# Performance work log

Hardware: AMD Instinct MI355X
Metric: run time of the kernel (lower is better)

The kernel has to match this reference:

```python
import jax, jax.numpy as jnp
import numpy as np

N_NODES = 1000
N_EDGES = 8000
IN_FEATS = 64
HID = 128
RDIM = HID // 2  # UniversalReadout output dim
EPS = 1e-5


def _lrelu(v):
    return jax.nn.leaky_relu(v, 0.01)


def setup_inputs() -> dict:
    key = jax.random.key(0)
    ks = jax.random.split(key, 16)
    B = 128
    node_feats = jax.random.normal(ks[0], (B * N_NODES, IN_FEATS), jnp.float32)
    edge_weights = jax.random.uniform(ks[1], (B * N_EDGES,), jnp.float32)
    g_weights = jax.random.uniform(ks[2], (B * N_NODES,), jnp.float32)
    src = jax.random.randint(ks[3], (N_EDGES,), 0, N_NODES)
    dst = jax.random.randint(ks[4], (N_EDGES,), 0, N_NODES)
    # GraphConv weights (in, out), kaiming-ish scale
    W1 = jax.random.normal(ks[5], (IN_FEATS, HID), jnp.float32) / np.sqrt(IN_FEATS)
    W2 = jax.random.normal(ks[6], (HID, HID), jnp.float32) / np.sqrt(HID)
    W3 = jax.random.normal(ks[7], (HID, HID), jnp.float32) / np.sqrt(HID)
    suppl = jnp.ones((3, N_EDGES), jnp.float32)           # suppl_weights_conv1..3
    AR = jnp.ones((4, N_NODES), jnp.float32)              # AR1..AR4 weights
    gn_gamma = jnp.ones((3, HID), jnp.float32)
    gn_beta = jnp.zeros((3, HID), jnp.float32)
    gn_alpha = jnp.ones((3, HID), jnp.float32)            # GraphNorm mean-scale
    phi_W = jax.random.normal(ks[8], (3, HID, HID), jnp.float32) / np.sqrt(HID)
    phi_b = jnp.zeros((3, HID), jnp.float32)
    rho_W = jax.random.normal(ks[9], (3, HID, RDIM), jnp.float32) / np.sqrt(HID)
    rho_b = jnp.zeros((3, RDIM), jnp.float32)
    return dict(node_feats=node_feats, edge_weights=edge_weights, g_weights=g_weights,
                W1=W1, W2=W2, W3=W3, suppl=suppl, AR=AR,
                gn_gamma=gn_gamma, gn_beta=gn_beta, gn_alpha=gn_alpha,
                phi_W=phi_W, phi_b=phi_b, rho_W=rho_W, rho_b=rho_b,
                src=src, dst=dst)


def _forward(node_feats, edge_weights, g_weights, W1, W2, W3, suppl, AR,
             gn_gamma, gn_beta, gn_alpha, phi_W, phi_b, rho_W, rho_b, src, dst):
    B = node_feats.shape[0] // N_NODES
    x = node_feats.reshape(B, N_NODES, -1)        # (B, N, F)
    gw = g_weights.reshape(B, N_NODES)            # (B, N)
    ew = edge_weights.reshape(B, N_EDGES)         # (B, E)

    # structural degree normalization (norm='both'), shared topology
    deg_out = jnp.maximum(jnp.zeros((N_NODES,), x.dtype).at[src].add(1.0), 1.0)
    deg_in = jnp.maximum(jnp.zeros((N_NODES,), x.dtype).at[dst].add(1.0), 1.0)
    n_out = deg_out ** -0.5
    n_in = deg_in ** -0.5

    def gconv(h, W, ew_l):
        hs = h * n_out[None, :, None]
        msgs = hs[:, src, :] * ew_l[:, :, None]                       # (B, E, D)
        agg = jnp.zeros_like(hs).at[:, dst].add(msgs)                  # scatter-add
        return (agg * n_in[None, :, None]) @ W

    def gnorm(h, i):
        mean = h.mean(axis=1, keepdims=True)
        sub = h - gn_alpha[i] * mean
        var = (sub * sub).mean(axis=1, keepdims=True)
        return gn_gamma[i] * sub * jax.lax.rsqrt(var + EPS) + gn_beta[i]

    def uro(h, i):  # UniversalReadout (deep-sets): per-node MLP -> sum -> MLP
        z = _lrelu(h @ phi_W[i] + phi_b[i]).sum(axis=1)
        return _lrelu(z @ rho_W[i] + rho_b[i])

    def wmean(h, ar):  # dgl.mean_nodes with node weight: mean over nodes of w*x
        w = gw * ar[None, :]
        return (w[:, :, None] * h).mean(axis=1)

    pieces = [wmean(x, AR[0])]
    h = x
    Ws = (W1, W2, W3)
    for i in range(3):
        h = _lrelu(gnorm(gconv(h, Ws[i], ew * suppl[i][None, :]), i))
        pieces.append(uro(h, i))
        pieces.append(wmean(h, AR[i + 1]))
    return _lrelu(jnp.concatenate(pieces, axis=-1))


def reference(node_feats, edge_weights, g_weights, W1, W2, W3, suppl, AR,
              gn_gamma, gn_beta, gn_alpha, phi_W, phi_b, rho_W, rho_b, src, dst):
    return _forward(node_feats, edge_weights, g_weights, W1, W2, W3, suppl, AR,
                    gn_gamma, gn_beta, gn_alpha, phi_W, phi_b, rho_W, rho_b, src, dst)
```

## Files before the change

### kernel.cpp

```cpp
#include <hip/hip_runtime.h>
#include <cstddef>

#define NN 1000
#define NE 8000
#define FIN 64
#define DH 128
#define RD 64
#define FEPS 1e-5f

typedef short short8 __attribute__((ext_vector_type(8)));
typedef float f32x4 __attribute__((ext_vector_type(4)));

__device__ __forceinline__ float lrelu(float x){ return x > 0.f ? x : 0.01f*x; }

__device__ __forceinline__ unsigned short f2b(float x){
  union { float f; unsigned int u; } v; v.f = x;
  unsigned int r = (v.u + 0x7fffu + ((v.u >> 16) & 1u)) >> 16;
  return (unsigned short)r;
}
__device__ __forceinline__ float b2f(unsigned int lo16){
  union { unsigned int u; float f; } v; v.u = lo16 << 16; return v.f;
}
__device__ __forceinline__ unsigned int pack2(float a, float b){
  return (unsigned int)f2b(a) | ((unsigned int)f2b(b) << 16);
}


__global__ __launch_bounds__(1024) void k_prep(const int* __restrict__ src,
        const int* __restrict__ dst,
        const float* __restrict__ W1, const float* __restrict__ W2,
        const float* __restrict__ W3, const float* __restrict__ phiW,
        unsigned short* __restrict__ wt,
        const float* __restrict__ x, const float* __restrict__ gw,
        const float* __restrict__ AR, float* __restrict__ out,
        float* nout, float* nin, int* rp, int* ord,
        int* csr_s, int* csr_e, int* csr_d, int B){
  __shared__ int sdo[1024], sdi[1024], ssc[1024], sfill[1024];
  __shared__ int hist[256], hoff[256];
  __shared__ float red2[16][64];
  int bid = blockIdx.x, t = threadIdx.x;

  if (bid == 0){
    sdo[t] = 0; sdi[t] = 0;
    __syncthreads();
    for (int e = t; e < NE; e += 1024){
      atomicAdd(&sdo[src[e]], 1);
      atomicAdd(&sdi[dst[e]], 1);
    }
    __syncthreads();
    int d = sdi[t];
    ssc[t] = d; __syncthreads();
    for (int off = 1; off < 1024; off <<= 1){
      int v = (t >= off) ? ssc[t-off] : 0;
      __syncthreads();
      ssc[t] += v;
      __syncthreads();
    }
    int myrp = ssc[t] - d;
    if (t < NN){
      rp[t] = myrp;
      nin[t]  = rsqrtf((float)max(sdi[t], 1));
      nout[t] = rsqrtf((float)max(sdo[t], 1));
    }
    if (t == NN-1) rp[NN] = ssc[t];
    sfill[t] = myrp;
    __syncthreads();
    for (int e = t; e < NE; e += 1024){
      int dn = dst[e];
      int pos = atomicAdd(&sfill[dn], 1);
      csr_s[pos] = src[e];
      csr_e[pos] = e;
      csr_d[pos] = dn;
    }
    if (t < 256) hist[t] = 0;
    __syncthreads();
    if (t < NN) atomicAdd(&hist[min(sdi[t], 255)], 1);
    __syncthreads();
    if (t < 256) hoff[t] = hist[t];
    __syncthreads();
    for (int off = 1; off < 256; off <<= 1){
      int v = (t < 256 && t >= off) ? hoff[t-off] : 0;
      __syncthreads();
      if (t < 256) hoff[t] += v;
      __syncthreads();
    }
    if (t < 256) hoff[t] -= hist[t];
    __syncthreads();
    if (t < NN){
      int pos = atomicAdd(&hoff[min(sdi[t], 255)], 1);
      ord[pos] = t;
    }
  } else if (bid <= 88){
    int i = (bid-1)*1024 + t;
    if (i < 8192){
      int n = i >> 6, k = i & 63;
      wt[i] = f2b(W1[k*128 + n]);
    } else if (i < 24576){
      int j = i - 8192; int n = j >> 7, k = j & 127;
      wt[i] = f2b(W2[k*128 + n]);
    } else if (i < 40960){
      int j = i - 24576; int n = j >> 7, k = j & 127;
      wt[i] = f2b(W3[k*128 + n]);
    } else {
      int j = i - 40960; int m = j >> 14; int jj = j & 16383;
      int n = jj >> 7, k = jj & 127;
      wt[i] = f2b(phiW[m*16384 + k*128 + n]);
    }
  } else {
    int b = bid - 89;
    int r = t >> 6, l = t & 63;
    float acc = 0.f;
    for (int v = r; v < NN; v += 16)
      acc += gw[(size_t)b*NN + v]*AR[v]*x[((size_t)b*NN + v)*FIN + l];
    red2[r][l] = acc;
    __syncthreads();
    if (t < 64){
      float s = 0.f;
      #pragma unroll
      for (int g2 = 0; g2 < 16; ++g2) s += red2[g2][t];
      out[(size_t)b*640 + t] = s*(1.f/NN);
    }
  }
}


__global__ __launch_bounds__(256) void k_edge(const float* __restrict__ ew,
        const float* __restrict__ sup, const float* __restrict__ nout,
        const float* __restrict__ nin, const int* __restrict__ csr_s,
        const int* __restrict__ csr_e, const int* __restrict__ csr_d,
        int2* __restrict__ ecl, float* __restrict__ statz, int nz4, int B){
  int bid = blockIdx.x, t = threadIdx.x;
  int gi = bid*256 + t;
  if (gi < nz4) ((float4*)statz)[gi] = make_float4(0.f,0.f,0.f,0.f);
  int layer, b, q;
  if ((B & 7) == 0){
    int xcd = bid & 7, r = bid >> 3;
    int bsub = r/12, rem = r - bsub*12;
    layer = rem >> 2; q = rem & 3; b = bsub*8 + xcd;
  } else {
    layer = bid/(4*B);
    int rem = bid - layer*4*B;
    b = rem >> 2; q = rem & 3;
  }
  const float* ewb  = ew  + (size_t)b*NE;
  const float* supl = sup + (size_t)layer*NE;
  int2* o = ecl + ((size_t)layer*B + b)*NE;
  for (int k = q*2000 + t; k < q*2000 + 2000; k += 256){
    int e = csr_e[k]; int s = csr_s[k];
    float wv = ewb[e]*supl[e]*nout[s]*nin[csr_d[k]];
    int2 v; v.x = s; v.y = __float_as_int(wv);
    o[k] = v;
  }
}


__global__ __launch_bounds__(256) void k_gathF(const float* __restrict__ x,
        const int2* __restrict__ ec, const int* __restrict__ rp,
        const int* __restrict__ ord, unsigned short* __restrict__ agg, int B){
  int bid = blockIdx.x;
  int b, chunk;
  if ((B & 7) == 0){
    int xcd = bid & 7, r = bid >> 3;
    int bsub = r/63; chunk = r - bsub*63; b = bsub*8 + xcd;
  } else { b = bid/63; chunk = bid - b*63; }
  int t = threadIdx.x;
  int grp = t >> 4, j = t & 15;
  int rk = chunk*16 + grp; if (rk > NN-1) rk = NN-1;
  int v = ord[rk];
  int kb = rp[v], ke = rp[v+1];
  const float* xb = x + (size_t)b*NN*FIN;
  const int2* ecb = ec + (size_t)b*NE;
  float acc[4][4] = {};
  int k = kb;
  for (; k+3 < ke; k += 4){
    #pragma unroll
    for (int uu = 0; uu < 4; ++uu){
      int2 e = ecb[k+uu];
      float4 xr = *(const float4*)(xb + e.x*FIN + j*4);
      float wgt = __int_as_float(e.y);
      acc[uu][0] = fmaf(xr.x, wgt, acc[uu][0]);
      acc[uu][1] = fmaf(xr.y, wgt, acc[uu][1]);
      acc[uu][2] = fmaf(xr.z, wgt, acc[uu][2]);
      acc[uu][3] = fmaf(xr.w, wgt, acc[uu][3]);
    }
  }
  for (; k < ke; ++k){
    int2 e = ecb[k];
    float4 xr = *(const float4*)(xb + e.x*FIN + j*4);
    float wgt = __int_as_float(e.y);
    acc[0][0] = fmaf(xr.x, wgt, acc[0][0]);
    acc[0][1] = fmaf(xr.y, wgt, acc[0][1]);
    acc[0][2] = fmaf(xr.z, wgt, acc[0][2]);
    acc[0][3] = fmaf(xr.w, wgt, acc[0][3]);
  }
  uint2 o;
  o.x = pack2(acc[0][0]+acc[1][0]+acc[2][0]+acc[3][0],
              acc[0][1]+acc[1][1]+acc[2][1]+acc[3][1]);
  o.y = pack2(acc[0][2]+acc[1][2]+acc[2][2]+acc[3][2],
              acc[0][3]+acc[1][3]+acc[2][3]+acc[3][3]);
  *(uint2*)(agg + ((size_t)b*NN + v)*FIN + j*4) = o;
}


__global__ __launch_bounds__(256) void k_gathB(const unsigned short* __restrict__ h,
        const int2* __restrict__ ec, const int* __restrict__ rp,
        const int* __restrict__ ord, unsigned short* __restrict__ agg, int B){
  int bid = blockIdx.x;
  int b, chunk;
  if ((B & 7) == 0){
    int xcd = bid & 7, r = bid >> 3;
    int bsub = r/63; chunk = r - bsub*63; b = bsub*8 + xcd;
  } else { b = bid/63; chunk = bid - b*63; }
  int t = threadIdx.x;
  int grp = t >> 4, j = t & 15;
  int rk = chunk*16 + grp; if (rk > NN-1) rk = NN-1;
  int v = ord[rk];
  int kb = rp[v], ke = rp[v+1];
  const unsigned short* hb = h + (size_t)b*NN*DH;
  const int2* ecb = ec + (size_t)b*NE;
  float acc[4][8] = {};
  int k = kb;
  for (; k+3 < ke; k += 4){
    #pragma unroll
    for (int uu = 0; uu < 4; ++uu){
      int2 e = ecb[k+uu];
      uint4 u = *(const uint4*)(hb + e.x*DH + j*8);
      float wgt = __int_as_float(e.y);
      acc[uu][0] = fmaf(b2f(u.x & 0xffffu), wgt, acc[uu][0]);
      acc[uu][1] = fmaf(b2f(u.x >> 16),     wgt, acc[uu][1]);
      acc[uu][2] = fmaf(b2f(u.y & 0xffffu), wgt, acc[uu][2]);
      acc[uu][3] = fmaf(b2f(u.y >> 16),     wgt, acc[uu][3]);
      acc[uu][4] = fmaf(b2f(u.z & 0xffffu), wgt, acc[uu][4]);
      acc[uu][5] = fmaf(b2f(u.z >> 16),     wgt, acc[uu][5]);
      acc[uu][6] = fmaf(b2f(u.w & 0xffffu), wgt, acc[uu][6]);
      acc[uu][7] = fmaf(b2f(u.w >> 16),     wgt, acc[uu][7]);
    }
  }
  for (; k < ke; ++k){
    int2 e = ecb[k];
    uint4 u = *(const uint4*)(hb + e.x*DH + j*8);
    float wgt = __int_as_float(e.y);
    acc[0][0] = fmaf(b2f(u.x & 0xffffu), wgt, acc[0][0]);
    acc[0][1] = fmaf(b2f(u.x >> 16),     wgt, acc[0][1]);
    acc[0][2] = fmaf(b2f(u.y & 0xffffu), wgt, acc[0][2]);
    acc[0][3] = fmaf(b2f(u.y >> 16),     wgt, acc[0][3]);
    acc[0][4] = fmaf(b2f(u.z & 0xffffu), wgt, acc[0][4]);
    acc[0][5] = fmaf(b2f(u.z >> 16),     wgt, acc[0][5]);
    acc[0][6] = fmaf(b2f(u.w & 0xffffu), wgt, acc[0][6]);
    acc[0][7] = fmaf(b2f(u.w >> 16),     wgt, acc[0][7]);
  }
  float f[8];
  #pragma unroll
  for (int d2 = 0; d2 < 8; ++d2)
    f[d2] = acc[0][d2]+acc[1][d2]+acc[2][d2]+acc[3][d2];
  uint4 o;
  o.x = pack2(f[0],f[1]); o.y = pack2(f[2],f[3]);
  o.z = pack2(f[4],f[5]); o.w = pack2(f[6],f[7]);
  *(uint4*)(agg + ((size_t)b*NN + v)*DH + j*8) = o;
}


template<int K>
__global__ __launch_bounds__(256) void k_conv(const unsigned short* __restrict__ A,
        const unsigned short* __restrict__ Wt, unsigned short* __restrict__ Cb,
        float* __restrict__ red_out, int B){
  constexpr int K2 = K*2;
  constexpr int CPR = K/8;
  __shared__ __align__(16) char smem[64*K2 + 128*K2];
  char* sA = smem;
  char* sW = smem + 64*K2;
  int t = threadIdx.x;
  int b, tile;
  if ((B & 7) == 0){
    int xcd = blockIdx.x & 7, r = blockIdx.x >> 3;
    int bsub = r >> 4; tile = r & 15; b = bsub*8 + xcd;
  } else { b = blockIdx.x >> 4; tile = blockIdx.x & 15; }
  int rows = NN - tile*64; if (rows > 64) rows = 64;
  size_t row0 = (size_t)b*NN + tile*64;
  size_t Mtot = (size_t)B*NN;

  for (int i = t; i < 64*CPR; i += 256){
    int r = i/CPR, cb = i%CPR;
    size_t gr = row0 + r; if (gr >= Mtot) gr = Mtot - 1;
    uint4 v = *(const uint4*)(A + gr*K + cb*8);
    *(uint4*)(sA + r*K2 + ((cb*16) ^ ((r & 7) << 4))) = v;
  }
  for (int i = t; i < 128*CPR; i += 256){
    int n = i/CPR, cb = i%CPR;
    uint4 v = *(const uint4*)(Wt + n*K + cb*8);
    *(uint4*)(sW + n*K2 + ((cb*16) ^ ((n & 7) << 4))) = v;
  }
  __syncthreads();

  int w = t >> 6, l = t & 63;
  int lr = l & 15, lk = l >> 4;
  f32x4 acc[8] = {};
  int arow = w*16 + lr;
  #pragma unroll
  for (int kk = 0; kk < K/32; ++kk){
    int kb = kk*64 + lk*16;
    short8 a = *(const short8*)(sA + arow*K2 + (kb ^ ((arow & 7) << 4)));
    #pragma unroll
    for (int f = 0; f < 8; ++f){
      int n = f*16 + lr;
      short8 bf = *(const short8*)(sW + n*K2 + (kb ^ ((n & 7) << 4)));
      acc[f] = __builtin_amdgcn_mfma_f32_16x16x32_bf16(a, bf, acc[f], 0, 0, 0);
    }
  }
  __syncthreads();

  float* red = (float*)smem;
  float cs[8], cq[8];
  int rbase = w*16 + lk*4;
  #pragma unroll
  for (int f = 0; f < 8; ++f){
    int col = f*16 + lr;
    float s = 0.f, q = 0.f;
    #pragma unroll
    for (int r = 0; r < 4; ++r){
      int row = rbase + r;
      bool ok = row < rows;
      float v = acc[f][r];
      if (ok) Cb[(row0 + row)*DH + col] = f2b(v);
      s += ok ? v : 0.f;
      q += ok ? v*v : 0.f;
    }
    s += __shfl_xor(s, 16); s += __shfl_xor(s, 32);
    q += __shfl_xor(q, 16); q += __shfl_xor(q, 32);
    cs[f] = s; cq[f] = q;
  }
  if (l < 16){
    #pragma unroll
    for (int f = 0; f < 8; ++f){
      red[w*128 + f*16 + l] = cs[f];
      red[512 + w*128 + f*16 + l] = cq[f];
    }
  }
  __syncthreads();
  if (t < 128){
    float s = red[t] + red[128+t] + red[256+t] + red[384+t];
    atomicAdd(&red_out[(size_t)b*DH + t], s);
    float q = red[512+t] + red[640+t] + red[768+t] + red[896+t];
    atomicAdd(&red_out[(size_t)B*DH + (size_t)b*DH + t], q);
  }
}


__global__ __launch_bounds__(256) void k_phi(const unsigned short* __restrict__ hpre,
        const unsigned short* __restrict__ Wt,
        const float* __restrict__ ssum, const float* __restrict__ ssq,
        const float* __restrict__ alpha, const float* __restrict__ gamma,
        const float* __restrict__ beta, const float* __restrict__ bias,
        const float* __restrict__ gw, const float* __restrict__ ar,
        unsigned short* __restrict__ hnorm,
        float* __restrict__ zout, float* __restrict__ out, int off, int B){
  __shared__ __align__(16) char smem[64*256 + 128*256];
  __shared__ __align__(16) float sivg[128], spc[128];
  __shared__ float sgw[64];
  char* sA = smem;
  char* sW = smem + 64*256;
  int t = threadIdx.x;
  int b, tile;
  if ((B & 7) == 0){
    int xcd = blockIdx.x & 7, r = blockIdx.x >> 3;
    int bsub = r >> 4; tile = r & 15; b = bsub*8 + xcd;
  } else { b = blockIdx.x >> 4; tile = blockIdx.x & 15; }
  int rows = NN - tile*64; if (rows > 64) rows = 64;
  size_t row0 = (size_t)b*NN + tile*64;

  if (t < 128){
    float m   = ssum[(size_t)b*DH + t]*(1.f/NN);
    float ex2 = ssq [(size_t)b*DH + t]*(1.f/NN);
    float a = alpha[t];
    float var = ex2 - (2.f*a - a*a)*m*m;
    float g = gamma[t]*rsqrtf(var + FEPS);
    sivg[t] = g;
    spc [t] = beta[t] - a*m*g;
  } else if (t < 192){
    int vr = tile*64 + (t - 128);
    sgw[t-128] = (vr < NN) ? gw[(size_t)b*NN + vr]*ar[vr] : 0.f;
  }
  __syncthreads();

  for (int i = t; i < 64*16; i += 256){
    int r = i >> 4, cb = i & 15;
    int rr = (r < rows) ? r : 0;
    uint4 u = *(const uint4*)(hpre + (row0 + rr)*DH + cb*8);
    int c0 = cb*8;
    float4 g1 = *(const float4*)(sivg + c0), g2 = *(const float4*)(sivg + c0 + 4);
    float4 p1 = *(const float4*)(spc + c0),  p2 = *(const float4*)(spc + c0 + 4);
    float xv[8];
    xv[0] = b2f(u.x & 0xffffu); xv[1] = b2f(u.x >> 16);
    xv[2] = b2f(u.y & 0xffffu); xv[3] = b2f(u.y >> 16);
    xv[4] = b2f(u.z & 0xffffu); xv[5] = b2f(u.z >> 16);
    xv[6] = b2f(u.w & 0xffffu); xv[7] = b2f(u.w >> 16);
    float gg[8] = {g1.x,g1.y,g1.z,g1.w,g2.x,g2.y,g2.z,g2.w};
    float pv[8] = {p1.x,p1.y,p1.z,p1.w,p2.x,p2.y,p2.z,p2.w};
    float nv[8];
    #pragma unroll
    for (int d2 = 0; d2 < 8; ++d2){
      float n0 = fmaf(xv[d2], gg[d2], pv[d2]);
      nv[d2] = fmaxf(n0, 0.01f*n0);
    }
    uint4 o;
    o.x = pack2(nv[0],nv[1]); o.y = pack2(nv[2],nv[3]);
    o.z = pack2(nv[4],nv[5]); o.w = pack2(nv[6],nv[7]);
    *(uint4*)(sA + r*256 + ((cb*16) ^ ((r & 7) << 4))) = o;
    if (hnorm != nullptr && r < rows)
      *(uint4*)(hnorm + (row0 + r)*DH + cb*8) = o;
  }
  for (int i = t; i < 128*16; i += 256){
    int n = i >> 4, cb = i & 15;
    uint4 v = *(const uint4*)(Wt + n*DH + cb*8);
    *(uint4*)(sW + n*256 + ((cb*16) ^ ((n & 7) << 4))) = v;
  }
  __syncthreads();

  int w = t >> 6, l = t & 63;
  int lr = l & 15, lk = l >> 4;
  f32x4 acc[8] = {};
  int arow = w*16 + lr;
  #pragma unroll
  for (int kk = 0; kk < 4; ++kk){
    int kb = kk*64 + lk*16;
    short8 a = *(const short8*)(sA + arow*256 + (kb ^ ((arow & 7) << 4)));
    #pragma unroll
    for (int f = 0; f < 8; ++f){
      int n = f*16 + lr;
      short8 bf = *(const short8*)(sW + n*256 + (kb ^ ((n & 7) << 4)));
      acc[f] = __builtin_amdgcn_mfma_f32_16x16x32_bf16(a, bf, acc[f], 0, 0, 0);
    }
  }
  __syncthreads();

  float* red = (float*)sW;
  float cs[8];
  int rbase = w*16 + lk*4;
  #pragma unroll
  for (int f = 0; f < 8; ++f){
    int col = f*16 + lr;
    float bv = bias[col];
    float s = 0.f;
    #pragma unroll
    for (int r = 0; r < 4; ++r){
      int row = rbase + r;
      float u = lrelu(acc[f][r] + bv);
      s += (row < rows) ? u : 0.f;
    }
    s += __shfl_xor(s, 16); s += __shfl_xor(s, 32);
    cs[f] = s;
  }
  if (l < 16){
    #pragma unroll
    for (int f = 0; f < 8; ++f) red[w*128 + f*16 + l] = cs[f];
  }
  __syncthreads();
  if (t < 128){
    float s = red[t] + red[128+t] + red[256+t] + red[384+t];
    atomicAdd(&zout[(size_t)b*DH + t], s);
  } else {
    int col = t - 128;
    float s = 0.f;
    for (int r = 0; r < 64; ++r){
      int byteoff = r*256 + (((col >> 3)*16) ^ ((r & 7) << 4)) + (col & 7)*2;
      s += sgw[r]*b2f(*(const unsigned short*)(sA + byteoff));
    }
    atomicAdd(&out[(size_t)b*640 + off + col], s*(1.f/NN));
  }
}


__global__ void k_final(const float* __restrict__ statz, const float* __restrict__ rhoW,
                        const float* __restrict__ rhob, float* __restrict__ out, int B){
  int b = blockIdx.x;
  int t = threadIdx.x;
  if (t < 192){
    int i = t >> 6, d = t & 63;
    const float* z = statz + ((size_t)i*3 + 2)*(size_t)B*DH + (size_t)b*DH;
    float acc = rhob[i*RD + d];
    const float* Wm = rhoW + (size_t)i*DH*RD;
    for (int k = 0; k < DH; ++k) acc = fmaf(z[k], Wm[k*RD + d], acc);
    out[(size_t)b*640 + 64 + i*192 + d] = lrelu(lrelu(acc));
  }
  for (int s = t; s < 448; s += 256){
    int idx;
    if (s < 64) idx = s;
    else { int j = s - 64; idx = 128 + (j >> 7)*192 + (j & 127); }
    size_t gi = (size_t)b*640 + idx;
    out[gi] = lrelu(out[gi]);
  }
}


extern "C" void kernel_launch(void* const* d_in, const int* in_sizes, int n_in,
                              void* d_out, int out_size, void* d_ws, size_t ws_size,
                              hipStream_t stream){
  const float* x    = (const float*)d_in[0];
  const float* ew   = (const float*)d_in[1];
  const float* gw   = (const float*)d_in[2];
  const float* W1   = (const float*)d_in[3];
  const float* W2   = (const float*)d_in[4];
  const float* W3   = (const float*)d_in[5];
  const float* sup  = (const float*)d_in[6];
  const float* AR   = (const float*)d_in[7];
  const float* gam  = (const float*)d_in[8];
  const float* bet  = (const float*)d_in[9];
  const float* alp  = (const float*)d_in[10];
  const float* phiW = (const float*)d_in[11];
  const float* phib = (const float*)d_in[12];
  const float* rhoW = (const float*)d_in[13];
  const float* rhob = (const float*)d_in[14];
  const int*   src  = (const int*)d_in[15];
  const int*   dst  = (const int*)d_in[16];
  float* out = (float*)d_out;

  int B = in_sizes[0] / (NN*FIN);
  size_t M = (size_t)B*NN;
  size_t BD = (size_t)B*DH;

  float* w = (float*)d_ws;
  size_t p = 0;
  float* nout = w+p; p += 1024;
  float* nin  = w+p; p += 1024;
  int* rp     = (int*)(w+p); p += 1024;
  int* ord    = (int*)(w+p); p += 1024;
  int* csr_s  = (int*)(w+p); p += 8192;
  int* csr_e  = (int*)(w+p); p += 8192;
  int* csr_d  = (int*)(w+p); p += 8192;
  float* statz = w+p; p += 3*3*BD;
  unsigned short* wt = (unsigned short*)(w+p); p += 45056;
  int2* ecl   = (int2*)(w+p); p += (size_t)6*B*NE;
  unsigned short* hpre  = (unsigned short*)(w+p); p += M*DH/2;
  unsigned short* hnorm = (unsigned short*)(w+p); p += M*DH/2;
  unsigned short* agg   = (unsigned short*)(w+p); p += M*DH/2;

  hipMemsetAsync(out, 0, (size_t)out_size*sizeof(float), stream);

  k_prep<<<89 + B, 1024, 0, stream>>>(src, dst, W1, W2, W3, phiW, wt,
      x, gw, AR, out, nout, nin, rp, ord, csr_s, csr_e, csr_d, B);
  k_edge<<<12*B, 256, 0, stream>>>(ew, sup, nout, nin, csr_s, csr_e, csr_d,
      ecl, statz, (int)(9*BD/4), B);

  const int wt_off[3] = {0, 8192, 24576};

  for (int i = 0; i < 3; ++i){
    float* SS = statz + (size_t)i*3*BD;
    if (i == 0){
      k_gathF<<<B*63, 256, 0, stream>>>(x, ecl, rp, ord, agg, B);
      k_conv<FIN><<<B*16, 256, 0, stream>>>(agg, wt, hpre, SS, B);
    } else {
      k_gathB<<<B*63, 256, 0, stream>>>(hnorm, ecl + (size_t)i*B*NE, rp, ord, agg, B);
      k_conv<DH><<<B*16, 256, 0, stream>>>(agg, wt + wt_off[i], hpre, SS, B);
    }
    k_phi<<<B*16, 256, 0, stream>>>(hpre, wt + 40960 + i*16384,
        SS, SS + BD, alp + i*DH, gam + i*DH, bet + i*DH, phib + i*DH,
        gw, AR + (size_t)(i+1)*NN, (i == 2) ? nullptr : hnorm,
        SS + 2*BD, out, 128 + i*192, B);
  }

  k_final<<<B, 256, 0, stream>>>(statz, rhoW, rhob, out, B);
}
```

Before: 268.5 us.

## Stage per-graph feature column slices in LDS for gather aggregation

The gather kernels now assign one block per (graph, quarter of feature columns). Each block first copies that column slice for all 1000 nodes into shared memory (64KB), then walks every destination node's CSR edges and reads source rows from LDS instead of scattered global loads. This replaces random global/L2 reads with a coalesced bulk load plus LDS gathers. In exchange, grid size drops to 4*B blocks with large LDS footprint, which limits occupancy, and each thread now writes narrow 2- or 4-byte outputs while re-reading the edge list once per column quarter.

```diff
diff --git a/kernel.cpp b/kernel.cpp
--- a/kernel.cpp
+++ b/kernel.cpp
@@ -154,109 +154,98 @@
 }
 
 
-__global__ __launch_bounds__(256) void k_gathF(const float* __restrict__ x,
+__global__ __launch_bounds__(512) void k_gathF(const float* __restrict__ x,
         const int2* __restrict__ ec, const int* __restrict__ rp,
         const int* __restrict__ ord, unsigned short* __restrict__ agg, int B){
+  __shared__ __align__(16) float sh[NN*16];
   int bid = blockIdx.x;
-  int b, chunk;
+  int b, q;
   if ((B & 7) == 0){
     int xcd = bid & 7, r = bid >> 3;
-    int bsub = r/63; chunk = r - bsub*63; b = bsub*8 + xcd;
-  } else { b = bid/63; chunk = bid - b*63; }
+    q = r & 3; b = (r >> 2)*8 + xcd;
+  } else { b = bid >> 2; q = bid & 3; }
   int t = threadIdx.x;
+  const float* xb = x + (size_t)b*NN*FIN + q*16;
+  for (int i = t; i < NN*4; i += 512){
+    int row = i >> 2, c = i & 3;
+    float4 v = *(const float4*)(xb + row*FIN + c*4);
+    *(float4*)(sh + row*16 + c*4) = v;
+  }
+  __syncthreads();
   int grp = t >> 4, j = t & 15;
-  int rk = chunk*16 + grp; if (rk > NN-1) rk = NN-1;
-  int v = ord[rk];
-  int kb = rp[v], ke = rp[v+1];
-  const float* xb = x + (size_t)b*NN*FIN;
   const int2* ecb = ec + (size_t)b*NE;
-  float acc[4][4] = {};
-  int k = kb;
-  for (; k+3 < ke; k += 4){
-    #pragma unroll
-    for (int uu = 0; uu < 4; ++uu){
-      int2 e = ecb[k+uu];
-      float4 xr = *(const float4*)(xb + e.x*FIN + j*4);
-      float wgt = __int_as_float(e.y);
-      acc[uu][0] = fmaf(xr.x, wgt, acc[uu][0]);
-      acc[uu][1] = fmaf(xr.y, wgt, acc[uu][1]);
-      acc[uu][2] = fmaf(xr.z, wgt, acc[uu][2]);
-      acc[uu][3] = fmaf(xr.w, wgt, acc[uu][3]);
-    }
-  }
-  for (; k < ke; ++k){
-    int2 e = ecb[k];
-    float4 xr = *(const float4*)(xb + e.x*FIN + j*4);
-    float wgt = __int_as_float(e.y);
-    acc[0][0] = fmaf(xr.x, wgt, acc[0][0]);
-    acc[0][1] = fmaf(xr.y, wgt, acc[0][1]);
-    acc[0][2] = fmaf(xr.z, wgt, acc[0][2]);
-    acc[0][3] = fmaf(xr.w, wgt, acc[0][3]);
-  }
-  uint2 o;
-  o.x = pack2(acc[0][0]+acc[1][0]+acc[2][0]+acc[3][0],
-              acc[0][1]+acc[1][1]+acc[2][1]+acc[3][1]);
-  o.y = pack2(acc[0][2]+acc[1][2]+acc[2][2]+acc[3][2],
-              acc[0][3]+acc[1][3]+acc[2][3]+acc[3][3]);
-  *(uint2*)(agg + ((size_t)b*NN + v)*FIN + j*4) = o;
-}
-
-
-__global__ __launch_bounds__(256) void k_gathB(const unsigned short* __restrict__ h,
+  for (int rk = grp; rk < NN; rk += 32){
+    int v = ord[rk];
+    int kb = rp[v], ke = rp[v+1];
+    float a0=0.f, a1=0.f, a2=0.f, a3=0.f;
+    int k = kb;
+    for (; k+3 < ke; k += 4){
+      int2 e0 = ecb[k], e1 = ecb[k+1], e2 = ecb[k+2], e3 = ecb[k+3];
+      a0 = fmaf(sh[e0.x*16 + j], __int_as_float(e0.y), a0);
+      a1 = fmaf(sh[e1.x*16 + j], __int_as_float(e1.y), a1);
+      a2 = fmaf(sh[e2.x*16 + j], __int_as_float(e2.y), a2);
+      a3 = fmaf(sh[e3.x*16 + j], __int_as_float(e3.y), a3);
+    }
+    for (; k < ke; ++k){
+      int2 e0 = ecb[k];
+      a0 = fmaf(sh[e0.x*16 + j], __int_as_float(e0.y), a0);
+    }
+    agg[((size_t)b*NN + v)*FIN + q*16 + j] = f2b(a0+a1+a2+a3);
+  }
+}
+
+
+__global__ __launch_bounds__(512) void k_gathB(const unsigned short* __restrict__ h,
         const int2* __restrict__ ec, const int* __restrict__ rp,
         const int* __restrict__ ord, unsigned short* __restrict__ agg, int B){
+  __shared__ __align__(16) unsigned shu[NN*16];
   int bid = blockIdx.x;
-  int b, chunk;
+  int b, q;
   if ((B & 7) == 0){
     int xcd = bid & 7, r = bid >> 3;
-    int bsub = r/63; chunk = r - bsub*63; b = bsub*8 + xcd;
-  } else { b = bid/63; chunk = bid - b*63; }
+    q = r & 3; b = (r >> 2)*8 + xcd;
+  } else { b = bid >> 2; q = bid & 3; }
   int t = threadIdx.x;
+  const unsigned short* hb = h + (size_t)b*NN*DH + q*32;
+  for (int i = t; i < NN*4; i += 512){
+    int row = i >> 2, c = i & 3;
+    uint4 v = *(const uint4*)(hb + row*DH + c*8);
+    *(uint4*)(shu + row*16 + c*4) = v;
+  }
+  __syncthreads();
   int grp = t >> 4, j = t & 15;
-  int rk = chunk*16 + grp; if (rk > NN-1) rk = NN-1;
-  int v = ord[rk];
-  int kb = rp[v], ke = rp[v+1];
-  const unsigned short* hb = h + (size_t)b*NN*DH;
   const int2* ecb = ec + (size_t)b*NE;
-  float acc[4][8] = {};
-  int k = kb;
-  for (; k+3 < ke; k += 4){
-    #pragma unroll
-    for (int uu = 0; uu < 4; ++uu){
-      int2 e = ecb[k+uu];
-      uint4 u = *(const uint4*)(hb + e.x*DH + j*8);
-      float wgt = __int_as_float(e.y);
-      acc[uu][0] = fmaf(b2f(u.x & 0xffffu), wgt, acc[uu][0]);
-      acc[uu][1] = fmaf(b2f(u.x >> 16),     wgt, acc[uu][1]);
-      acc[uu][2] = fmaf(b2f(u.y & 0xffffu), wgt, acc[uu][2]);
-      acc[uu][3] = fmaf(b2f(u.y >> 16),     wgt, acc[uu][3]);
-      acc[uu][4] = fmaf(b2f(u.z & 0xffffu), wgt, acc[uu][4]);
-      acc[uu][5] = fmaf(b2f(u.z >> 16),     wgt, acc[uu][5]);
-      acc[uu][6] = fmaf(b2f(u.w & 0xffffu), wgt, acc[uu][6]);
-      acc[uu][7] = fmaf(b2f(u.w >> 16),     wgt, acc[uu][7]);
-    }
-  }
-  for (; k < ke; ++k){
-    int2 e = ecb[k];
-    uint4 u = *(const uint4*)(hb + e.x*DH + j*8);
-    float wgt = __int_as_float(e.y);
-    acc[0][0] = fmaf(b2f(u.x & 0xffffu), wgt, acc[0][0]);
-    acc[0][1] = fmaf(b2f(u.x >> 16),     wgt, acc[0][1]);
-    acc[0][2] = fmaf(b2f(u.y & 0xffffu), wgt, acc[0][2]);
-    acc[0][3] = fmaf(b2f(u.y >> 16),     wgt, acc[0][3]);
-    acc[0][4] = fmaf(b2f(u.z & 0xffffu), wgt, acc[0][4]);
-    acc[0][5] = fmaf(b2f(u.z >> 16),     wgt, acc[0][5]);
-    acc[0][6] = fmaf(b2f(u.w & 0xffffu), wgt, acc[0][6]);
-    acc[0][7] = fmaf(b2f(u.w >> 16),     wgt, acc[0][7]);
-  }
-  float f[8];
-  #pragma unroll
-  for (int d2 = 0; d2 < 8; ++d2)
-    f[d2] = acc[0][d2]+acc[1][d2]+acc[2][d2]+acc[3][d2];
-  uint4 o;
-  o.x = pack2(f[0],f[1]); o.y = pack2(f[2],f[3]);
-  o.z = pack2(f[4],f[5]); o.w = pack2(f[6],f[7]);
-  *(uint4*)(agg + ((size_t)b*NN + v)*DH + j*8) = o;
+  for (int rk = grp; rk < NN; rk += 32){
+    int v = ord[rk];
+    int kb = rp[v], ke = rp[v+1];
+    float a[4][2] = {};
+    int k = kb;
+    for (; k+3 < ke; k += 4){
+      int2 e0 = ecb[k], e1 = ecb[k+1], e2 = ecb[k+2], e3 = ecb[k+3];
+      unsigned u0 = shu[e0.x*16 + j], u1 = shu[e1.x*16 + j];
+      unsigned u2 = shu[e2.x*16 + j], u3 = shu[e3.x*16 + j];
+      float w0 = __int_as_float(e0.y), w1 = __int_as_float(e1.y);
+      float w2 = __int_as_float(e2.y), w3 = __int_as_float(e3.y);
+      a[0][0] = fmaf(b2f(u0 & 0xffffu), w0, a[0][0]);
+      a[0][1] = fmaf(b2f(u0 >> 16),     w0, a[0][1]);
+      a[1][0] = fmaf(b2f(u1 & 0xffffu), w1, a[1][0]);
+      a[1][1] = fmaf(b2f(u1 >> 16),     w1, a[1][1]);
+      a[2][0] = fmaf(b2f(u2 & 0xffffu), w2, a[2][0]);
+      a[2][1] = fmaf(b2f(u2 >> 16),     w2, a[2][1]);
+      a[3][0] = fmaf(b2f(u3 & 0xffffu), w3, a[3][0]);
+      a[3][1] = fmaf(b2f(u3 >> 16),     w3, a[3][1]);
+    }
+    for (; k < ke; ++k){
+      int2 e0 = ecb[k];
+      unsigned u0 = shu[e0.x*16 + j];
+      float w0 = __int_as_float(e0.y);
+      a[0][0] = fmaf(b2f(u0 & 0xffffu), w0, a[0][0]);
+      a[0][1] = fmaf(b2f(u0 >> 16),     w0, a[0][1]);
+    }
+    unsigned o = pack2(a[0][0]+a[1][0]+a[2][0]+a[3][0],
+                       a[0][1]+a[1][1]+a[2][1]+a[3][1]);
+    *(unsigned*)(agg + ((size_t)b*NN + v)*DH + q*32 + j*2) = o;
+  }
 }
 
 
@@ -546,10 +535,10 @@
   for (int i = 0; i < 3; ++i){
     float* SS = statz + (size_t)i*3*BD;
     if (i == 0){
-      k_gathF<<<B*63, 256, 0, stream>>>(x, ecl, rp, ord, agg, B);
+      k_gathF<<<4*B, 512, 0, stream>>>(x, ecl, rp, ord, agg, B);
       k_conv<FIN><<<B*16, 256, 0, stream>>>(agg, wt, hpre, SS, B);
     } else {
-      k_gathB<<<B*63, 256, 0, stream>>>(hnorm, ecl + (size_t)i*B*NE, rp, ord, agg, B);
+      k_gathB<<<4*B, 512, 0, stream>>>(hnorm, ecl + (size_t)i*B*NE, rp, ord, agg, B);
       k_conv<DH><<<B*16, 256, 0, stream>>>(agg, wt + wt_off[i], hpre, SS, B);
     }
     k_phi<<<B*16, 256, 0, stream>>>(hpre, wt + 40960 + i*16384,
```

Result: slower. 353.4 us (+31.7%).

## Split conv and phi GEMM tiles across two output-column halves

Applied to the files above, without the earlier changes.

The conv and phi kernels now launch twice as many blocks, and each block computes 64 of the 128 output columns instead of all of them. This halves per-block shared memory and accumulator registers and doubles the grid, aiming for higher occupancy and more parallelism. The cost is that each A tile is loaded twice, and in phi the normalization of the A tile is recomputed by both halves. The hnorm store and the weighted-mean readout in phi run only in the first half.

```diff
diff --git a/kernel.cpp b/kernel.cpp
--- a/kernel.cpp
+++ b/kernel.cpp
@@ -266,15 +266,18 @@
         float* __restrict__ red_out, int B){
   constexpr int K2 = K*2;
   constexpr int CPR = K/8;
-  __shared__ __align__(16) char smem[64*K2 + 128*K2];
+  __shared__ __align__(16) char smem[64*K2 + 64*K2];
   char* sA = smem;
   char* sW = smem + 64*K2;
   int t = threadIdx.x;
-  int b, tile;
+  int b, tile, cb2;
   if ((B & 7) == 0){
     int xcd = blockIdx.x & 7, r = blockIdx.x >> 3;
-    int bsub = r >> 4; tile = r & 15; b = bsub*8 + xcd;
-  } else { b = blockIdx.x >> 4; tile = blockIdx.x & 15; }
+    int tc = r & 31; tile = tc >> 1; cb2 = tc & 1;
+    b = (r >> 5)*8 + xcd;
+  } else {
+    int r = blockIdx.x; b = r >> 5; int tc = r & 31; tile = tc >> 1; cb2 = tc & 1;
+  }
   int rows = NN - tile*64; if (rows > 64) rows = 64;
   size_t row0 = (size_t)b*NN + tile*64;
   size_t Mtot = (size_t)B*NN;
@@ -285,23 +288,23 @@
     uint4 v = *(const uint4*)(A + gr*K + cb*8);
     *(uint4*)(sA + r*K2 + ((cb*16) ^ ((r & 7) << 4))) = v;
   }
-  for (int i = t; i < 128*CPR; i += 256){
+  for (int i = t; i < 64*CPR; i += 256){
     int n = i/CPR, cb = i%CPR;
-    uint4 v = *(const uint4*)(Wt + n*K + cb*8);
+    uint4 v = *(const uint4*)(Wt + (size_t)(cb2*64 + n)*K + cb*8);
     *(uint4*)(sW + n*K2 + ((cb*16) ^ ((n & 7) << 4))) = v;
   }
   __syncthreads();
 
   int w = t >> 6, l = t & 63;
   int lr = l & 15, lk = l >> 4;
-  f32x4 acc[8] = {};
+  f32x4 acc[4] = {};
   int arow = w*16 + lr;
   #pragma unroll
   for (int kk = 0; kk < K/32; ++kk){
     int kb = kk*64 + lk*16;
     short8 a = *(const short8*)(sA + arow*K2 + (kb ^ ((arow & 7) << 4)));
     #pragma unroll
-    for (int f = 0; f < 8; ++f){
+    for (int f = 0; f < 4; ++f){
       int n = f*16 + lr;
       short8 bf = *(const short8*)(sW + n*K2 + (kb ^ ((n & 7) << 4)));
       acc[f] = __builtin_amdgcn_mfma_f32_16x16x32_bf16(a, bf, acc[f], 0, 0, 0);
@@ -310,11 +313,11 @@
   __syncthreads();
 
   float* red = (float*)smem;
-  float cs[8], cq[8];
+  float cs[4], cq[4];
   int rbase = w*16 + lk*4;
   #pragma unroll
-  for (int f = 0; f < 8; ++f){
-    int col = f*16 + lr;
+  for (int f = 0; f < 4; ++f){
+    int col = cb2*64 + f*16 + lr;
     float s = 0.f, q = 0.f;
     #pragma unroll
     for (int r = 0; r < 4; ++r){
@@ -331,17 +334,17 @@
   }
   if (l < 16){
     #pragma unroll
-    for (int f = 0; f < 8; ++f){
-      red[w*128 + f*16 + l] = cs[f];
-      red[512 + w*128 + f*16 + l] = cq[f];
+    for (int f = 0; f < 4; ++f){
+      red[w*64 + f*16 + l] = cs[f];
+      red[256 + w*64 + f*16 + l] = cq[f];
     }
   }
   __syncthreads();
-  if (t < 128){
-    float s = red[t] + red[128+t] + red[256+t] + red[384+t];
-    atomicAdd(&red_out[(size_t)b*DH + t], s);
-    float q = red[512+t] + red[640+t] + red[768+t] + red[896+t];
-    atomicAdd(&red_out[(size_t)B*DH + (size_t)b*DH + t], q);
+  if (t < 64){
+    float s = red[t] + red[64+t] + red[128+t] + red[192+t];
+    atomicAdd(&red_out[(size_t)b*DH + cb2*64 + t], s);
+    float q = red[256+t] + red[320+t] + red[384+t] + red[448+t];
+    atomicAdd(&red_out[(size_t)B*DH + (size_t)b*DH + cb2*64 + t], q);
   }
 }
 
@@ -354,17 +357,21 @@
         const float* __restrict__ gw, const float* __restrict__ ar,
         unsigned short* __restrict__ hnorm,
         float* __restrict__ zout, float* __restrict__ out, int off, int B){
-  __shared__ __align__(16) char smem[64*256 + 128*256];
+  __shared__ __align__(16) char smem[64*256 + 64*256];
+  __shared__ __align__(16) float red[256];
   __shared__ __align__(16) float sivg[128], spc[128];
   __shared__ float sgw[64];
   char* sA = smem;
   char* sW = smem + 64*256;
   int t = threadIdx.x;
-  int b, tile;
+  int b, tile, cb2;
   if ((B & 7) == 0){
     int xcd = blockIdx.x & 7, r = blockIdx.x >> 3;
-    int bsub = r >> 4; tile = r & 15; b = bsub*8 + xcd;
-  } else { b = blockIdx.x >> 4; tile = blockIdx.x & 15; }
+    int tc = r & 31; tile = tc >> 1; cb2 = tc & 1;
+    b = (r >> 5)*8 + xcd;
+  } else {
+    int r = blockIdx.x; b = r >> 5; int tc = r & 31; tile = tc >> 1; cb2 = tc & 1;
+  }
   int rows = NN - tile*64; if (rows > 64) rows = 64;
   size_t row0 = (size_t)b*NN + tile*64;
 
@@ -406,39 +413,37 @@
     o.x = pack2(nv[0],nv[1]); o.y = pack2(nv[2],nv[3]);
     o.z = pack2(nv[4],nv[5]); o.w = pack2(nv[6],nv[7]);
     *(uint4*)(sA + r*256 + ((cb*16) ^ ((r & 7) << 4))) = o;
-    if (hnorm != nullptr && r < rows)
+    if (cb2 == 0 && hnorm != nullptr && r < rows)
       *(uint4*)(hnorm + (row0 + r)*DH + cb*8) = o;
   }
-  for (int i = t; i < 128*16; i += 256){
+  for (int i = t; i < 64*16; i += 256){
     int n = i >> 4, cb = i & 15;
-    uint4 v = *(const uint4*)(Wt + n*DH + cb*8);
+    uint4 v = *(const uint4*)(Wt + (size_t)(cb2*64 + n)*DH + cb*8);
     *(uint4*)(sW + n*256 + ((cb*16) ^ ((n & 7) << 4))) = v;
   }
   __syncthreads();
 
   int w = t >> 6, l = t & 63;
   int lr = l & 15, lk = l >> 4;
-  f32x4 acc[8] = {};
+  f32x4 acc[4] = {};
   int arow = w*16 + lr;
   #pragma unroll
   for (int kk = 0; kk < 4; ++kk){
     int kb = kk*64 + lk*16;
     short8 a = *(const short8*)(sA + arow*256 + (kb ^ ((arow & 7) << 4)));
     #pragma unroll
-    for (int f = 0; f < 8; ++f){
+    for (int f = 0; f < 4; ++f){
       int n = f*16 + lr;
       short8 bf = *(const short8*)(sW + n*256 + (kb ^ ((n & 7) << 4)));
       acc[f] = __builtin_amdgcn_mfma_f32_16x16x32_bf16(a, bf, acc[f], 0, 0, 0);
     }
   }
-  __syncthreads();
-
-  float* red = (float*)sW;
-  float cs[8];
+
+  float cs[4];
   int rbase = w*16 + lk*4;
   #pragma unroll
-  for (int f = 0; f < 8; ++f){
-    int col = f*16 + lr;
+  for (int f = 0; f < 4; ++f){
+    int col = cb2*64 + f*16 + lr;
     float bv = bias[col];
     float s = 0.f;
     #pragma unroll
@@ -452,14 +457,14 @@
   }
   if (l < 16){
     #pragma unroll
-    for (int f = 0; f < 8; ++f) red[w*128 + f*16 + l] = cs[f];
+    for (int f = 0; f < 4; ++f) red[w*64 + f*16 + l] = cs[f];
   }
   __syncthreads();
-  if (t < 128){
-    float s = red[t] + red[128+t] + red[256+t] + red[384+t];
-    atomicAdd(&zout[(size_t)b*DH + t], s);
-  } else {
-    int col = t - 128;
+  if (t < 64){
+    float s = red[t] + red[64+t] + red[128+t] + red[192+t];
+    atomicAdd(&zout[(size_t)b*DH + cb2*64 + t], s);
+  } else if (cb2 == 0 && t >= 64 && t < 192){
+    int col = t - 64;
     float s = 0.f;
     for (int r = 0; r < 64; ++r){
       int byteoff = r*256 + (((col >> 3)*16) ^ ((r & 7) << 4)) + (col & 7)*2;
@@ -547,12 +552,12 @@
     float* SS = statz + (size_t)i*3*BD;
     if (i == 0){
       k_gathF<<<B*63, 256, 0, stream>>>(x, ecl, rp, ord, agg, B);
-      k_conv<FIN><<<B*16, 256, 0, stream>>>(agg, wt, hpre, SS, B);
+      k_conv<FIN><<<B*32, 256, 0, stream>>>(agg, wt, hpre, SS, B);
     } else {
       k_gathB<<<B*63, 256, 0, stream>>>(hnorm, ecl + (size_t)i*B*NE, rp, ord, agg, B);
-      k_conv<DH><<<B*16, 256, 0, stream>>>(agg, wt + wt_off[i], hpre, SS, B);
-    }
-    k_phi<<<B*16, 256, 0, stream>>>(hpre, wt + 40960 + i*16384,
+      k_conv<DH><<<B*32, 256, 0, stream>>>(agg, wt + wt_off[i], hpre, SS, B);
+    }
+    k_phi<<<B*32, 256, 0, stream>>>(hpre, wt + 40960 + i*16384,
         SS, SS + BD, alp + i*DH, gam + i*DH, bet + i*DH, phib + i*DH,
         gw, AR + (size_t)(i+1)*NN, (i == 2) ? nullptr : hnorm,
         SS + 2*BD, out, 128 + i*192, B);
```

After: 275.4 us. +2.6%, slower.
